# Performance work log

Hardware: AMD Instinct MI355X
Metric: run time of the kernel (lower is better)

Reference implementation:

```python
import jax, jax.numpy as jnp
import numpy as np

E = 600000
NF = 50000
NC = 12500
D = 128
HID = 128
D_IN = 4 * D  # concat of four gathered feature blocks


def setup_inputs() -> dict:
    key = jax.random.key(0)
    ks = jax.random.split(key, 10)
    return {
        "h_dk_coarse": jax.random.normal(ks[0], (NC, D), dtype=jnp.float32),
        "h_si_fine": jax.random.normal(ks[1], (NF, D), dtype=jnp.float32),
        "h_sk_coarse": jax.random.normal(ks[2], (NC, D), dtype=jnp.float32),
        "h_di_fine_current": jax.random.normal(ks[3], (NF, D), dtype=jnp.float32),
        "fine_idx": jax.random.randint(ks[4], (E,), 0, NF, dtype=jnp.int64),
        "coarse_idx": jax.random.randint(ks[5], (E,), 0, NC, dtype=jnp.int64),
        # Dense params (Glorot-ish scale); both layers use relu per create_mlp
        "W1": jax.random.normal(ks[6], (D_IN, HID), dtype=jnp.float32) * (1.0 / np.sqrt(D_IN)),
        "b1": jnp.zeros((HID,), dtype=jnp.float32),
        "W2": jax.random.normal(ks[7], (HID, D), dtype=jnp.float32) * (1.0 / np.sqrt(HID)),
        "b2": jnp.zeros((D,), dtype=jnp.float32),
    }


def reference(h_dk_coarse, h_si_fine, h_sk_coarse, h_di_fine_current,
              fine_idx, coarse_idx, W1, b1, W2, b2):
    # Gather per-edge features
    h_dk_g = h_dk_coarse[coarse_idx]          # [E, D]
    h_si_g = h_si_fine[fine_idx]              # [E, D]
    h_sk_g = h_sk_coarse[coarse_idx]          # [E, D]
    h_di_g = h_di_fine_current[fine_idx]      # [E, D]
    x = jnp.concatenate([h_si_g, h_sk_g, h_di_g, h_dk_g], axis=-1)  # [E, 4D]
    # MLP: relu on hidden AND final layer (create_mlp default activation, no final override)
    h = jax.nn.relu(x @ W1 + b1)              # [E, HID]
    psi = jax.nn.relu(h @ W2 + b2)            # [E, D]
    contributions = psi * h_dk_g              # [E, D]
    # Scatter-add back to fine nodes
    return jax.ops.segment_sum(contributions, fine_idx, num_segments=NF)  # [NF, D]
```

## Files before the change

### kernel.cpp

```cpp
#include <hip/hip_runtime.h>

typedef unsigned char u8;
typedef unsigned short u16;
typedef unsigned int u32;

#define E_EDGES 600000
#define NUM_FINE 50000
#define NUM_COARSE 12500
#define FINE_BLOCKS 391
#define COARSE_BLOCKS 98
#define CONVERT_BLOCKS 320
#define HCONV_BLOCKS 782
#define COUNT_BLOCKS 2344
#define SCATTER_BLOCKS 2344
#define ZOUT_BLOCKS 625
#define PADF 53248
#define SCAN_BLOCKS 196

typedef __attribute__((ext_vector_type(8))) short short8;
typedef __attribute__((ext_vector_type(4))) float f32x4;

union Frag { short8 v; u16 s[8]; u32 u[4]; uint4 q; };

__device__ __forceinline__ u32 rne_bf16(float f) {
  union { float f; u32 u; } v; v.f = f;
  return (v.u + 0x7FFFu + ((v.u >> 16) & 1u)) >> 16;
}
__device__ __forceinline__ float hi_bf(u32 u) {
  union { u32 x; float f; } v; v.x = u & 0xFFFF0000u; return v.f;
}
__device__ __forceinline__ float lo_bf(u32 u) {
  union { u32 x; float f; } v; v.x = u << 16; return v.f;
}
__device__ __forceinline__ float up_bf(u16 u) {
  union { u32 x; float f; } v; v.x = ((u32)u) << 16; return v.f;
}
__device__ __forceinline__ u32 pack_trunc(float hi, float lo) {
  union { float f; u32 x; } a, b; a.f = hi; b.f = lo;
  return __builtin_amdgcn_perm(a.x, b.x, 0x07060302u);
}
__device__ __forceinline__ u32 addrelu_pack(u32 a, u32 b) {
  float lo = fmaxf(lo_bf(a) + lo_bf(b), 0.0f);
  float hi = fmaxf(hi_bf(a) + hi_bf(b), 0.0f);
  return pack_trunc(hi, lo);
}
__device__ __forceinline__ u16 trunc_bf16(float f) {
  union { float f; u32 u; } v; v.f = f;
  return (u16)(v.u >> 16);
}
__device__ __forceinline__ u32 rne_pack(float lo, float hi) {
  return rne_bf16(lo) | (rne_bf16(hi) << 16);
}

__global__ void prep1(const float* __restrict__ W1, const float* __restrict__ W2,
                      u16* __restrict__ BW1f, u16* __restrict__ BW1c,
                      u16* __restrict__ BW2,
                      const float* __restrict__ h_dk, u16* __restrict__ Hc,
                      const int* __restrict__ fidx, u32* __restrict__ cnt4,
                      u8* __restrict__ rk) {
  if (blockIdx.x < CONVERT_BLOCKS) {
    int o = blockIdx.x * 256 + threadIdx.x;
    if (o >= 81920) return;
    int which = (o < 32768) ? 0 : (o < 65536 ? 1 : 2);
    int idx = (which == 2) ? (o - 65536) : (o & 32767);
    int j = idx & 7, lane = (idx >> 3) & 63, nt = (idx >> 9) & 7, ks = idx >> 12;
    int k = ks * 32 + (lane >> 4) * 8 + j;
    int n = nt * 16 + (lane & 15);
    float v;
    if (which == 2) v = W2[k * 128 + n];
    else {
      int row;
      if (which == 0) row = (k < 128) ? k : (256 + (k - 128));
      else            row = (k < 128) ? (128 + k) : (384 + (k - 128));
      v = W1[row * 128 + n];
    }
    u16 b = (u16)rne_bf16(v);
    if (which == 0) BW1f[idx] = b; else if (which == 1) BW1c[idx] = b; else BW2[idx] = b;
  } else if (blockIdx.x < CONVERT_BLOCKS + HCONV_BLOCKS) {
    int t = (blockIdx.x - CONVERT_BLOCKS) * 256 + threadIdx.x;
    if (t < (NUM_COARSE * 128) / 8) {
      const float4* s = (const float4*)(h_dk + t * 8);
      float4 v0 = s[0], v1 = s[1];
      uint4 o;
      o.x = rne_pack(v0.x, v0.y);
      o.y = rne_pack(v0.z, v0.w);
      o.z = rne_pack(v1.x, v1.y);
      o.w = rne_pack(v1.z, v1.w);
      *(uint4*)(Hc + t * 8) = o;
    }
  } else {
    int e = (blockIdx.x - CONVERT_BLOCKS - HCONV_BLOCKS) * 256 + threadIdx.x;
    if (e < E_EDGES) {
      int fi = fidx[e];
      u32 r = atomicAdd(&cnt4[(e & 3) * PADF + fi], 1u);
      rk[e] = (u8)r;
    }
  }
}

__global__ void scan1(const u32* __restrict__ cnt4, u32* __restrict__ roots) {
  __shared__ u32 wsum[4];
  const int tid = threadIdx.x, lane = tid & 63, w = tid >> 6;
  const int fi = blockIdx.x * 256 + tid;
  u32 tot = 0;
  if (fi < NUM_FINE)
    tot = cnt4[fi] + cnt4[PADF + fi] + cnt4[2 * PADF + fi] + cnt4[3 * PADF + fi];
  u32 x = tot;
#pragma unroll
  for (int off = 32; off >= 1; off >>= 1) x += __shfl_down(x, off, 64);
  if (lane == 0) wsum[w] = x;
  __syncthreads();
  if (tid == 0) roots[blockIdx.x] = wsum[0] + wsum[1] + wsum[2] + wsum[3];
}

__global__ void scan2(u32* __restrict__ cnt4, const u32* __restrict__ roots) {
  __shared__ u32 wsum[4], wred[4];
  __shared__ u32 sh_bbase;
  const int tid = threadIdx.x, lane = tid & 63, w = tid >> 6;
  const int fi = blockIdx.x * 256 + tid;

  u32 c0 = 0, c1 = 0, c2 = 0, c3 = 0;
  if (fi < NUM_FINE) {
    c0 = cnt4[fi];            c1 = cnt4[PADF + fi];
    c2 = cnt4[2 * PADF + fi]; c3 = cnt4[3 * PADF + fi];
  }
  const u32 tot = c0 + c1 + c2 + c3;

  u32 rv = (tid < (int)blockIdx.x && tid < SCAN_BLOCKS) ? roots[tid] : 0;
#pragma unroll
  for (int off = 32; off >= 1; off >>= 1) rv += __shfl_down(rv, off, 64);
  if (lane == 0) wred[w] = rv;
  __syncthreads();
  if (tid == 0) sh_bbase = wred[0] + wred[1] + wred[2] + wred[3];

  u32 xi = tot;
#pragma unroll
  for (int off = 1; off < 64; off <<= 1) {
    u32 y = __shfl_up(xi, off, 64);
    if (lane >= off) xi += y;
  }
  if (lane == 63) wsum[w] = xi;
  __syncthreads();
  u32 woffs = 0;
  for (int k = 0; k < w; ++k) woffs += wsum[k];
  const u32 g = sh_bbase + woffs + xi - tot;

  if (fi < NUM_FINE) {
    cnt4[fi] = g;
    cnt4[PADF + fi] = g + c0;
    cnt4[2 * PADF + fi] = g + c0 + c1;
    cnt4[3 * PADF + fi] = g + c0 + c1 + c2;
  }
}

__global__ __launch_bounds__(256, 2) void prep2(
    const int* __restrict__ fidx, const int* __restrict__ cidx,
    const u32* __restrict__ base4, const u8* __restrict__ rk,
    u32* __restrict__ spk, float* __restrict__ out,
    const float* __restrict__ h_dk, const float* __restrict__ h_si,
    const float* __restrict__ h_sk, const float* __restrict__ h_di,
    const u16* __restrict__ BW1f, const u16* __restrict__ BW1c,
    const float* __restrict__ b1, u16* __restrict__ Pf, u16* __restrict__ Pc) {
  __shared__ u16 bsh[32768];

  if (blockIdx.x < SCATTER_BLOCKS) {
    int e = blockIdx.x * 256 + threadIdx.x;
    if (e < E_EDGES) {
      int fi = fidx[e];
      u32 pos = base4[(e & 3) * PADF + fi] + rk[e];
      spk[pos] = ((u32)fi << 14) | (u32)cidx[e];
    }
    return;
  }
  if (blockIdx.x < SCATTER_BLOCKS + ZOUT_BLOCKS) {
    const int zb = blockIdx.x - SCATTER_BLOCKS;
    float4* o4 = (float4*)out;
    const float4 z = {0.f, 0.f, 0.f, 0.f};
    int idx = zb * 2560 + threadIdx.x;
#pragma unroll
    for (int i = 0; i < 10; ++i) o4[idx + i * 256] = z;
    return;
  }

  const int b = blockIdx.x - SCATTER_BLOCKS - ZOUT_BLOCKS;
  const bool fine = b < FINE_BLOCKS;
  const int rowStart = fine ? b * 128 : (b - FINE_BLOCKS) * 128;
  const int R = fine ? NUM_FINE : NUM_COARSE;
  const float* __restrict__ X1 = fine ? h_si : h_sk;
  const float* __restrict__ X2 = fine ? h_di : h_dk;
  const u16* __restrict__ BW = fine ? BW1f : BW1c;
  u16* __restrict__ P = fine ? Pf : Pc;

  const int tid = threadIdx.x;
  {
    uint4* d4 = (uint4*)bsh;
    const uint4* s4 = (const uint4*)BW;
#pragma unroll
    for (int k = 0; k < 16; ++k) d4[k * 256 + tid] = s4[k * 256 + tid];
  }
  __syncthreads();

  const int lane = tid & 63;
  const int w = tid >> 6;
  const int qd = lane >> 4;
  const int ml = lane & 15;

  int rowA[2]; bool vA[2];
#pragma unroll
  for (int mt = 0; mt < 2; ++mt) {
    rowA[mt] = rowStart + w * 32 + mt * 16 + ml;
    vA[mt] = rowA[mt] < R;
  }

  f32x4 acc[2][8];
#pragma unroll
  for (int mt = 0; mt < 2; ++mt)
#pragma unroll
    for (int nt = 0; nt < 8; ++nt) acc[mt][nt] = (f32x4){0.f, 0.f, 0.f, 0.f};

  for (int ks = 0; ks < 8; ++ks) {
    const int k0 = ks * 32 + qd * 8;
    short8 a[2];
#pragma unroll
    for (int mt = 0; mt < 2; ++mt) {
      Frag af;
      if (vA[mt]) {
        const float* src = (k0 < 128) ? (X1 + rowA[mt] * 128 + k0)
                                      : (X2 + rowA[mt] * 128 + (k0 - 128));
        const float4* s4 = (const float4*)src;
        float4 v0 = s4[0], v1 = s4[1];
        af.u[0] = pack_trunc(v0.y, v0.x);
        af.u[1] = pack_trunc(v0.w, v0.z);
        af.u[2] = pack_trunc(v1.y, v1.x);
        af.u[3] = pack_trunc(v1.w, v1.z);
      } else {
        af.u[0] = af.u[1] = af.u[2] = af.u[3] = 0u;
      }
      a[mt] = af.v;
    }
#pragma unroll
    for (int nt = 0; nt < 8; ++nt) {
      Frag bfr;
      bfr.q = *(const uint4*)&bsh[(((ks * 8 + nt) * 64) + lane) * 8];
      acc[0][nt] = __builtin_amdgcn_mfma_f32_16x16x32_bf16(a[0], bfr.v, acc[0][nt], 0, 0, 0);
      acc[1][nt] = __builtin_amdgcn_mfma_f32_16x16x32_bf16(a[1], bfr.v, acc[1][nt], 0, 0, 0);
    }
  }

  float b1v[8];
#pragma unroll
  for (int nt = 0; nt < 8; ++nt) b1v[nt] = fine ? 0.0f : b1[nt * 16 + ml];

#pragma unroll
  for (int mt = 0; mt < 2; ++mt) {
#pragma unroll
    for (int r = 0; r < 4; ++r) {
      const int row = rowStart + w * 32 + mt * 16 + qd * 4 + r;
      if (row < R) {
#pragma unroll
        for (int nt = 0; nt < 8; ++nt)
          P[row * 128 + nt * 16 + ml] = (u16)rne_bf16(acc[mt][nt][r] + b1v[nt]);
      }
    }
  }
}

__global__ __launch_bounds__(256, 4) void edge_kernel(
    const u16* __restrict__ Pf, const u16* __restrict__ Pc,
    const u16* __restrict__ BW2, const u16* __restrict__ Hc,
    const u32* __restrict__ spk, const float* __restrict__ b2,
    float* __restrict__ out) {
  __shared__ u16 smem[16384];
  __shared__ int sh_fi[128], sh_ci[128], sh_segstart[130];
  __shared__ int shS, shHead, shTail, shW0tot;

  const int tid = threadIdx.x;
  const int eb = blockIdx.x * 128;
  const int V = min(128, E_EDGES - eb);

  {
    uint4* d4 = (uint4*)smem;
    const uint4* s4 = (const uint4*)BW2;
#pragma unroll
    for (int k = 0; k < 8; ++k) d4[k * 256 + tid] = s4[k * 256 + tid];
  }
  if (tid < 128) {
    if (tid < V) {
      u32 p = spk[eb + tid];
      sh_fi[tid] = (int)(p >> 14);
      sh_ci[tid] = (int)(p & 16383u);
    } else { sh_fi[tid] = -1; sh_ci[tid] = 0; }
  }
  if (tid == 0) {
    shHead = (eb > 0) ? (int)(spk[eb - 1] >> 14) : -1;
    shTail = (eb + V < E_EDGES) ? (int)(spk[eb + V] >> 14) : -1;
  }
  __syncthreads();

  int f = 0, x = 0;
  if (tid < 128) {
    f = (tid < V) ? ((tid == 0) ? 1 : (sh_fi[tid] != sh_fi[tid - 1] ? 1 : 0)) : 0;
    x = f;
#pragma unroll
    for (int off = 1; off < 64; off <<= 1) {
      int y = __shfl_up(x, off, 64);
      if ((tid & 63) >= off) x += y;
    }
  }
  if (tid == 63) shW0tot = x;
  __syncthreads();
  if (tid >= 64 && tid < 128) x += shW0tot;
  if (tid < V) {
    if (f) sh_segstart[x - 1] = tid;
    if (tid == V - 1) { shS = x; sh_segstart[x] = V; }
  }
  __syncthreads();

  const int lane = tid & 63;
  const int w = tid >> 6;
  const int qd = lane >> 4;
  const int ml = lane & 15;

  int fiA[2], ciA[2]; bool vA[2];
#pragma unroll
  for (int mt = 0; mt < 2; ++mt) {
    const int lr = w * 32 + mt * 16 + ml;
    vA[mt] = lr < V;
    fiA[mt] = vA[mt] ? sh_fi[lr] : 0;
    ciA[mt] = vA[mt] ? sh_ci[lr] : 0;
  }

  f32x4 acc[2][8];
#pragma unroll
  for (int mt = 0; mt < 2; ++mt)
#pragma unroll
    for (int nt = 0; nt < 8; ++nt) acc[mt][nt] = (f32x4){0.f, 0.f, 0.f, 0.f};

  for (int ks = 0; ks < 4; ++ks) {
    const int k0 = ks * 32 + qd * 8;
    short8 a[2];
#pragma unroll
    for (int mt = 0; mt < 2; ++mt) {
      Frag af;
      if (vA[mt]) {
        uint4 pf = *(const uint4*)(Pf + fiA[mt] * 128 + k0);
        uint4 pc = *(const uint4*)(Pc + ciA[mt] * 128 + k0);
        af.u[0] = addrelu_pack(pf.x, pc.x);
        af.u[1] = addrelu_pack(pf.y, pc.y);
        af.u[2] = addrelu_pack(pf.z, pc.z);
        af.u[3] = addrelu_pack(pf.w, pc.w);
      } else {
        af.u[0] = af.u[1] = af.u[2] = af.u[3] = 0u;
      }
      a[mt] = af.v;
    }
#pragma unroll
    for (int nt = 0; nt < 8; ++nt) {
      Frag bfr;
      bfr.q = *(const uint4*)&smem[(((ks * 8 + nt) * 64) + lane) * 8];
      acc[0][nt] = __builtin_amdgcn_mfma_f32_16x16x32_bf16(a[0], bfr.v, acc[0][nt], 0, 0, 0);
      acc[1][nt] = __builtin_amdgcn_mfma_f32_16x16x32_bf16(a[1], bfr.v, acc[1][nt], 0, 0, 0);
    }
  }
  __syncthreads();

  float b2v[8];
#pragma unroll
  for (int nt = 0; nt < 8; ++nt) b2v[nt] = b2[nt * 16 + ml];

#pragma unroll
  for (int mt = 0; mt < 2; ++mt) {
#pragma unroll
    for (int r = 0; r < 4; ++r) {
      const int lr = w * 32 + mt * 16 + qd * 4 + r;
      if (lr < V) {
        const u16* __restrict__ hrow = Hc + sh_ci[lr] * 128;
#pragma unroll
        for (int nt = 0; nt < 8; ++nt) {
          const int col = nt * 16 + ml;
          const float psi = fmaxf(acc[mt][nt][r] + b2v[nt], 0.0f);
          smem[lr * 128 + col] = trunc_bf16(psi * up_bf(hrow[col]));
        }
      }
    }
  }
  __syncthreads();

  const int S = shS;
  for (int idx = tid; idx < S * 64; idx += 256) {
    const int s = idx >> 6, cp = idx & 63;
    const int r0 = sh_segstart[s], r1 = sh_segstart[s + 1];
    float a0 = 0.f, a1 = 0.f;
    for (int r = r0; r < r1; ++r) {
      const u32 v = *(const u32*)&smem[r * 128 + cp * 2];
      a0 += lo_bf(v);
      a1 += hi_bf(v);
    }
    const int fi = sh_fi[r0];
    float* op = out + (size_t)fi * 128 + cp * 2;
    const bool at = (s == 0 && shHead == fi) || (s == S - 1 && shTail == fi);
    if (at) { atomicAdd(op, a0); atomicAdd(op + 1, a1); }
    else { op[0] = a0; op[1] = a1; }
  }
}

extern "C" void kernel_launch(void* const* d_in, const int* in_sizes, int n_in,
                              void* d_out, int out_size, void* d_ws, size_t ws_size,
                              hipStream_t stream) {
  const float* h_dk = (const float*)d_in[0];
  const float* h_si = (const float*)d_in[1];
  const float* h_sk = (const float*)d_in[2];
  const float* h_di = (const float*)d_in[3];
  const int* fidx = (const int*)d_in[4];
  const int* cidx = (const int*)d_in[5];
  const float* W1 = (const float*)d_in[6];
  const float* b1 = (const float*)d_in[7];
  const float* W2 = (const float*)d_in[8];
  const float* b2 = (const float*)d_in[9];
  float* out = (float*)d_out;

  u16* Pf   = (u16*)d_ws;
  u16* Pc   = Pf + (size_t)NUM_FINE * 128;
  u16* BW1f = Pc + (size_t)NUM_COARSE * 128;
  u16* BW1c = BW1f + 32768;
  u16* BW2  = BW1c + 32768;
  u16* Hc   = BW2 + 16384;
  u32* cnt4 = (u32*)(Hc + (size_t)NUM_COARSE * 128);
  u32* spk  = cnt4 + 4 * PADF;
  u8*  rk   = (u8*)(spk + E_EDGES);
  u32* roots = (u32*)(rk + E_EDGES);

  hipMemsetAsync(cnt4, 0, 4 * PADF * sizeof(u32), stream);

  prep1<<<CONVERT_BLOCKS + HCONV_BLOCKS + COUNT_BLOCKS, 256, 0, stream>>>(
      W1, W2, BW1f, BW1c, BW2, h_dk, Hc, fidx, cnt4, rk);
  scan1<<<SCAN_BLOCKS, 256, 0, stream>>>(cnt4, roots);
  scan2<<<SCAN_BLOCKS, 256, 0, stream>>>(cnt4, roots);
  prep2<<<SCATTER_BLOCKS + ZOUT_BLOCKS + FINE_BLOCKS + COARSE_BLOCKS, 256, 0, stream>>>(
      fidx, cidx, cnt4, rk, spk, out, h_dk, h_si, h_sk, h_di,
      BW1f, BW1c, b1, Pf, Pc);
  edge_kernel<<<(E_EDGES + 127) / 128, 256, 0, stream>>>(
      Pf, Pc, BW2, Hc, spk, b2, out);
}
```

Baseline: 239.7 us.

## Move node-level GEMM into first kernel and convert W1 in-block

The per-node W1 projection (Pf/Pc) now runs in the first launch alongside the edge-count atomics and h_dk/W2 conversion, instead of after the scan in prep2. Each GEMM block converts its own half of W1 to bf16 into shared memory rather than reading a pre-converted copy, which drops a dependency stage and halves the shared-memory footprint. Counter copies for the atomic histogram grow from 4 to 8 to reduce contention. The cost is redundant W1 conversion in every GEMM block and more counter traffic in the scans.

```diff
diff --git a/kernel.cpp b/kernel.cpp
--- a/kernel.cpp
+++ b/kernel.cpp
@@ -9,12 +9,14 @@
 #define NUM_COARSE 12500
 #define FINE_BLOCKS 391
 #define COARSE_BLOCKS 98
-#define CONVERT_BLOCKS 320
+#define COUNT_BLOCKS 2344
+#define PRE_BLOCKS (FINE_BLOCKS + COARSE_BLOCKS)
 #define HCONV_BLOCKS 782
-#define COUNT_BLOCKS 2344
+#define W2CONV_BLOCKS 64
 #define SCATTER_BLOCKS 2344
 #define ZOUT_BLOCKS 625
 #define PADF 53248
+#define NCOPY 8
 #define SCAN_BLOCKS 196
 
 typedef __attribute__((ext_vector_type(8))) short short8;
@@ -52,153 +54,58 @@
   return rne_bf16(lo) | (rne_bf16(hi) << 16);
 }
 
-__global__ void prep1(const float* __restrict__ W1, const float* __restrict__ W2,
-                      u16* __restrict__ BW1f, u16* __restrict__ BW1c,
-                      u16* __restrict__ BW2,
-                      const float* __restrict__ h_dk, u16* __restrict__ Hc,
-                      const int* __restrict__ fidx, u32* __restrict__ cnt4,
-                      u8* __restrict__ rk) {
-  if (blockIdx.x < CONVERT_BLOCKS) {
-    int o = blockIdx.x * 256 + threadIdx.x;
-    if (o >= 81920) return;
-    int which = (o < 32768) ? 0 : (o < 65536 ? 1 : 2);
-    int idx = (which == 2) ? (o - 65536) : (o & 32767);
-    int j = idx & 7, lane = (idx >> 3) & 63, nt = (idx >> 9) & 7, ks = idx >> 12;
-    int k = ks * 32 + (lane >> 4) * 8 + j;
-    int n = nt * 16 + (lane & 15);
-    float v;
-    if (which == 2) v = W2[k * 128 + n];
-    else {
-      int row;
-      if (which == 0) row = (k < 128) ? k : (256 + (k - 128));
-      else            row = (k < 128) ? (128 + k) : (384 + (k - 128));
-      v = W1[row * 128 + n];
-    }
-    u16 b = (u16)rne_bf16(v);
-    if (which == 0) BW1f[idx] = b; else if (which == 1) BW1c[idx] = b; else BW2[idx] = b;
-  } else if (blockIdx.x < CONVERT_BLOCKS + HCONV_BLOCKS) {
-    int t = (blockIdx.x - CONVERT_BLOCKS) * 256 + threadIdx.x;
-    if (t < (NUM_COARSE * 128) / 8) {
-      const float4* s = (const float4*)(h_dk + t * 8);
-      float4 v0 = s[0], v1 = s[1];
-      uint4 o;
-      o.x = rne_pack(v0.x, v0.y);
-      o.y = rne_pack(v0.z, v0.w);
-      o.z = rne_pack(v1.x, v1.y);
-      o.w = rne_pack(v1.z, v1.w);
-      *(uint4*)(Hc + t * 8) = o;
-    }
-  } else {
-    int e = (blockIdx.x - CONVERT_BLOCKS - HCONV_BLOCKS) * 256 + threadIdx.x;
+__global__ __launch_bounds__(256, 2) void mega1(
+    const int* __restrict__ fidx, u32* __restrict__ cnt8, u8* __restrict__ rk,
+    const float* __restrict__ h_dk, const float* __restrict__ h_si,
+    const float* __restrict__ h_sk, const float* __restrict__ h_di,
+    const float* __restrict__ W1, const float* __restrict__ W2,
+    const float* __restrict__ b1,
+    u16* __restrict__ Pf, u16* __restrict__ Pc,
+    u16* __restrict__ Hc, u16* __restrict__ BW2) {
+  __shared__ u16 bsh[16384];
+
+  const int tid = threadIdx.x;
+
+  if (blockIdx.x < COUNT_BLOCKS) {
+    int e = blockIdx.x * 256 + tid;
     if (e < E_EDGES) {
       int fi = fidx[e];
-      u32 r = atomicAdd(&cnt4[(e & 3) * PADF + fi], 1u);
+      u32 r = atomicAdd(&cnt8[(e & 7) * PADF + fi], 1u);
       rk[e] = (u8)r;
     }
-  }
-}
-
-__global__ void scan1(const u32* __restrict__ cnt4, u32* __restrict__ roots) {
-  __shared__ u32 wsum[4];
-  const int tid = threadIdx.x, lane = tid & 63, w = tid >> 6;
-  const int fi = blockIdx.x * 256 + tid;
-  u32 tot = 0;
-  if (fi < NUM_FINE)
-    tot = cnt4[fi] + cnt4[PADF + fi] + cnt4[2 * PADF + fi] + cnt4[3 * PADF + fi];
-  u32 x = tot;
-#pragma unroll
-  for (int off = 32; off >= 1; off >>= 1) x += __shfl_down(x, off, 64);
-  if (lane == 0) wsum[w] = x;
-  __syncthreads();
-  if (tid == 0) roots[blockIdx.x] = wsum[0] + wsum[1] + wsum[2] + wsum[3];
-}
-
-__global__ void scan2(u32* __restrict__ cnt4, const u32* __restrict__ roots) {
-  __shared__ u32 wsum[4], wred[4];
-  __shared__ u32 sh_bbase;
-  const int tid = threadIdx.x, lane = tid & 63, w = tid >> 6;
-  const int fi = blockIdx.x * 256 + tid;
-
-  u32 c0 = 0, c1 = 0, c2 = 0, c3 = 0;
-  if (fi < NUM_FINE) {
-    c0 = cnt4[fi];            c1 = cnt4[PADF + fi];
-    c2 = cnt4[2 * PADF + fi]; c3 = cnt4[3 * PADF + fi];
-  }
-  const u32 tot = c0 + c1 + c2 + c3;
-
-  u32 rv = (tid < (int)blockIdx.x && tid < SCAN_BLOCKS) ? roots[tid] : 0;
-#pragma unroll
-  for (int off = 32; off >= 1; off >>= 1) rv += __shfl_down(rv, off, 64);
-  if (lane == 0) wred[w] = rv;
-  __syncthreads();
-  if (tid == 0) sh_bbase = wred[0] + wred[1] + wred[2] + wred[3];
-
-  u32 xi = tot;
-#pragma unroll
-  for (int off = 1; off < 64; off <<= 1) {
-    u32 y = __shfl_up(xi, off, 64);
-    if (lane >= off) xi += y;
-  }
-  if (lane == 63) wsum[w] = xi;
-  __syncthreads();
-  u32 woffs = 0;
-  for (int k = 0; k < w; ++k) woffs += wsum[k];
-  const u32 g = sh_bbase + woffs + xi - tot;
-
-  if (fi < NUM_FINE) {
-    cnt4[fi] = g;
-    cnt4[PADF + fi] = g + c0;
-    cnt4[2 * PADF + fi] = g + c0 + c1;
-    cnt4[3 * PADF + fi] = g + c0 + c1 + c2;
-  }
-}
-
-__global__ __launch_bounds__(256, 2) void prep2(
-    const int* __restrict__ fidx, const int* __restrict__ cidx,
-    const u32* __restrict__ base4, const u8* __restrict__ rk,
-    u32* __restrict__ spk, float* __restrict__ out,
-    const float* __restrict__ h_dk, const float* __restrict__ h_si,
-    const float* __restrict__ h_sk, const float* __restrict__ h_di,
-    const u16* __restrict__ BW1f, const u16* __restrict__ BW1c,
-    const float* __restrict__ b1, u16* __restrict__ Pf, u16* __restrict__ Pc) {
-  __shared__ u16 bsh[32768];
-
-  if (blockIdx.x < SCATTER_BLOCKS) {
-    int e = blockIdx.x * 256 + threadIdx.x;
-    if (e < E_EDGES) {
-      int fi = fidx[e];
-      u32 pos = base4[(e & 3) * PADF + fi] + rk[e];
-      spk[pos] = ((u32)fi << 14) | (u32)cidx[e];
-    }
     return;
   }
-  if (blockIdx.x < SCATTER_BLOCKS + ZOUT_BLOCKS) {
-    const int zb = blockIdx.x - SCATTER_BLOCKS;
-    float4* o4 = (float4*)out;
-    const float4 z = {0.f, 0.f, 0.f, 0.f};
-    int idx = zb * 2560 + threadIdx.x;
-#pragma unroll
-    for (int i = 0; i < 10; ++i) o4[idx + i * 256] = z;
+  if (blockIdx.x >= COUNT_BLOCKS + PRE_BLOCKS) {
+    const int bb = blockIdx.x - COUNT_BLOCKS - PRE_BLOCKS;
+    if (bb < HCONV_BLOCKS) {
+      int t = bb * 256 + tid;
+      if (t < (NUM_COARSE * 128) / 8) {
+        const float4* s = (const float4*)(h_dk + t * 8);
+        float4 v0 = s[0], v1 = s[1];
+        uint4 o;
+        o.x = rne_pack(v0.x, v0.y);
+        o.y = rne_pack(v0.z, v0.w);
+        o.z = rne_pack(v1.x, v1.y);
+        o.w = rne_pack(v1.z, v1.w);
+        *(uint4*)(Hc + t * 8) = o;
+      }
+    } else {
+      int idx = (bb - HCONV_BLOCKS) * 256 + tid;
+      int j = idx & 7, lane = (idx >> 3) & 63, nt = (idx >> 9) & 7, ks = idx >> 12;
+      int k = ks * 32 + (lane >> 4) * 8 + j;
+      int n = nt * 16 + (lane & 15);
+      BW2[idx] = (u16)rne_bf16(W2[k * 128 + n]);
+    }
     return;
   }
 
-  const int b = blockIdx.x - SCATTER_BLOCKS - ZOUT_BLOCKS;
+  const int b = blockIdx.x - COUNT_BLOCKS;
   const bool fine = b < FINE_BLOCKS;
   const int rowStart = fine ? b * 128 : (b - FINE_BLOCKS) * 128;
   const int R = fine ? NUM_FINE : NUM_COARSE;
   const float* __restrict__ X1 = fine ? h_si : h_sk;
   const float* __restrict__ X2 = fine ? h_di : h_dk;
-  const u16* __restrict__ BW = fine ? BW1f : BW1c;
   u16* __restrict__ P = fine ? Pf : Pc;
-
-  const int tid = threadIdx.x;
-  {
-    uint4* d4 = (uint4*)bsh;
-    const uint4* s4 = (const uint4*)BW;
-#pragma unroll
-    for (int k = 0; k < 16; ++k) d4[k * 256 + tid] = s4[k * 256 + tid];
-  }
-  __syncthreads();
 
   const int lane = tid & 63;
   const int w = tid >> 6;
@@ -218,33 +125,55 @@
 #pragma unroll
     for (int nt = 0; nt < 8; ++nt) acc[mt][nt] = (f32x4){0.f, 0.f, 0.f, 0.f};
 
-  for (int ks = 0; ks < 8; ++ks) {
-    const int k0 = ks * 32 + qd * 8;
-    short8 a[2];
-#pragma unroll
-    for (int mt = 0; mt < 2; ++mt) {
-      Frag af;
-      if (vA[mt]) {
-        const float* src = (k0 < 128) ? (X1 + rowA[mt] * 128 + k0)
-                                      : (X2 + rowA[mt] * 128 + (k0 - 128));
-        const float4* s4 = (const float4*)src;
-        float4 v0 = s4[0], v1 = s4[1];
-        af.u[0] = pack_trunc(v0.y, v0.x);
-        af.u[1] = pack_trunc(v0.w, v0.z);
-        af.u[2] = pack_trunc(v1.y, v1.x);
-        af.u[3] = pack_trunc(v1.w, v1.z);
-      } else {
-        af.u[0] = af.u[1] = af.u[2] = af.u[3] = 0u;
-      }
-      a[mt] = af.v;
-    }
-#pragma unroll
-    for (int nt = 0; nt < 8; ++nt) {
-      Frag bfr;
-      bfr.q = *(const uint4*)&bsh[(((ks * 8 + nt) * 64) + lane) * 8];
-      acc[0][nt] = __builtin_amdgcn_mfma_f32_16x16x32_bf16(a[0], bfr.v, acc[0][nt], 0, 0, 0);
-      acc[1][nt] = __builtin_amdgcn_mfma_f32_16x16x32_bf16(a[1], bfr.v, acc[1][nt], 0, 0, 0);
-    }
+  for (int half = 0; half < 2; ++half) {
+    {
+      const int kl = tid >> 1;
+      const int nh = (tid & 1) * 64;
+      const int wrow = (fine ? 0 : 128) + half * 256 + kl;
+      const float4* __restrict__ src = (const float4*)(W1 + wrow * 128 + nh);
+      const int ksl = kl >> 5, kqd = (kl >> 3) & 3, j = kl & 7;
+#pragma unroll 4
+      for (int g4 = 0; g4 < 16; ++g4) {
+        float4 v = src[g4];
+        const int n = nh + g4 * 4;
+        const int nt = n >> 4;
+        u16* dst = &bsh[(((ksl * 8 + nt) * 64) + kqd * 16 + (n & 15)) * 8 + j];
+        dst[0]  = (u16)rne_bf16(v.x);
+        dst[8]  = (u16)rne_bf16(v.y);
+        dst[16] = (u16)rne_bf16(v.z);
+        dst[24] = (u16)rne_bf16(v.w);
+      }
+    }
+    __syncthreads();
+
+    const float* __restrict__ X = half ? X2 : X1;
+    for (int ksl = 0; ksl < 4; ++ksl) {
+      const int k0 = ksl * 32 + qd * 8;
+      short8 a[2];
+#pragma unroll
+      for (int mt = 0; mt < 2; ++mt) {
+        Frag af;
+        if (vA[mt]) {
+          const float4* s4 = (const float4*)(X + rowA[mt] * 128 + k0);
+          float4 v0 = s4[0], v1 = s4[1];
+          af.u[0] = pack_trunc(v0.y, v0.x);
+          af.u[1] = pack_trunc(v0.w, v0.z);
+          af.u[2] = pack_trunc(v1.y, v1.x);
+          af.u[3] = pack_trunc(v1.w, v1.z);
+        } else {
+          af.u[0] = af.u[1] = af.u[2] = af.u[3] = 0u;
+        }
+        a[mt] = af.v;
+      }
+#pragma unroll
+      for (int nt = 0; nt < 8; ++nt) {
+        Frag bfr;
+        bfr.q = *(const uint4*)&bsh[(((ksl * 8 + nt) * 64) + lane) * 8];
+        acc[0][nt] = __builtin_amdgcn_mfma_f32_16x16x32_bf16(a[0], bfr.v, acc[0][nt], 0, 0, 0);
+        acc[1][nt] = __builtin_amdgcn_mfma_f32_16x16x32_bf16(a[1], bfr.v, acc[1][nt], 0, 0, 0);
+      }
+    }
+    __syncthreads();
   }
 
   float b1v[8];
@@ -262,6 +191,82 @@
           P[row * 128 + nt * 16 + ml] = (u16)rne_bf16(acc[mt][nt][r] + b1v[nt]);
       }
     }
+  }
+}
+
+__global__ void scan1(const u32* __restrict__ cnt8, u32* __restrict__ roots) {
+  __shared__ u32 wsum[4];
+  const int tid = threadIdx.x, lane = tid & 63, w = tid >> 6;
+  const int fi = blockIdx.x * 256 + tid;
+  u32 tot = 0;
+  if (fi < NUM_FINE) {
+#pragma unroll
+    for (int c = 0; c < NCOPY; ++c) tot += cnt8[c * PADF + fi];
+  }
+  u32 x = tot;
+#pragma unroll
+  for (int off = 32; off >= 1; off >>= 1) x += __shfl_down(x, off, 64);
+  if (lane == 0) wsum[w] = x;
+  __syncthreads();
+  if (tid == 0) roots[blockIdx.x] = wsum[0] + wsum[1] + wsum[2] + wsum[3];
+}
+
+__global__ void scan2(u32* __restrict__ cnt8, const u32* __restrict__ roots) {
+  __shared__ u32 wsum[4], wred[4];
+  __shared__ u32 sh_bbase;
+  const int tid = threadIdx.x, lane = tid & 63, w = tid >> 6;
+  const int fi = blockIdx.x * 256 + tid;
+
+  u32 c[NCOPY];
+  u32 tot = 0;
+#pragma unroll
+  for (int i = 0; i < NCOPY; ++i) {
+    c[i] = (fi < NUM_FINE) ? cnt8[i * PADF + fi] : 0;
+    tot += c[i];
+  }
+
+  u32 rv = (tid < (int)blockIdx.x && tid < SCAN_BLOCKS) ? roots[tid] : 0;
+#pragma unroll
+  for (int off = 32; off >= 1; off >>= 1) rv += __shfl_down(rv, off, 64);
+  if (lane == 0) wred[w] = rv;
+  __syncthreads();
+  if (tid == 0) sh_bbase = wred[0] + wred[1] + wred[2] + wred[3];
+
+  u32 xi = tot;
+#pragma unroll
+  for (int off = 1; off < 64; off <<= 1) {
+    u32 y = __shfl_up(xi, off, 64);
+    if (lane >= off) xi += y;
+  }
+  if (lane == 63) wsum[w] = xi;
+  __syncthreads();
+  u32 woffs = 0;
+  for (int k = 0; k < w; ++k) woffs += wsum[k];
+  u32 g = sh_bbase + woffs + xi - tot;
+
+  if (fi < NUM_FINE) {
+#pragma unroll
+    for (int i = 0; i < NCOPY; ++i) { cnt8[i * PADF + fi] = g; g += c[i]; }
+  }
+}
+
+__global__ void scatterz(const int* __restrict__ fidx, const int* __restrict__ cidx,
+                         const u32* __restrict__ base8, const u8* __restrict__ rk,
+                         u32* __restrict__ spk, float* __restrict__ out) {
+  if (blockIdx.x < SCATTER_BLOCKS) {
+    int e = blockIdx.x * 256 + threadIdx.x;
+    if (e < E_EDGES) {
+      int fi = fidx[e];
+      u32 pos = base8[(e & 7) * PADF + fi] + rk[e];
+      spk[pos] = ((u32)fi << 14) | (u32)cidx[e];
+    }
+  } else {
+    const int zb = blockIdx.x - SCATTER_BLOCKS;
+    float4* o4 = (float4*)out;
+    const float4 z = {0.f, 0.f, 0.f, 0.f};
+    int idx = zb * 2560 + threadIdx.x;
+#pragma unroll
+    for (int i = 0; i < 10; ++i) o4[idx + i * 256] = z;
   }
 }
 
@@ -421,24 +426,21 @@
 
   u16* Pf   = (u16*)d_ws;
   u16* Pc   = Pf + (size_t)NUM_FINE * 128;
-  u16* BW1f = Pc + (size_t)NUM_COARSE * 128;
-  u16* BW1c = BW1f + 32768;
-  u16* BW2  = BW1c + 32768;
+  u16* BW2  = Pc + (size_t)NUM_COARSE * 128;
   u16* Hc   = BW2 + 16384;
-  u32* cnt4 = (u32*)(Hc + (size_t)NUM_COARSE * 128);
-  u32* spk  = cnt4 + 4 * PADF;
+  u32* cnt8 = (u32*)(Hc + (size_t)NUM_COARSE * 128);
+  u32* spk  = cnt8 + NCOPY * PADF;
   u8*  rk   = (u8*)(spk + E_EDGES);
   u32* roots = (u32*)(rk + E_EDGES);
 
-  hipMemsetAsync(cnt4, 0, 4 * PADF * sizeof(u32), stream);
-
-  prep1<<<CONVERT_BLOCKS + HCONV_BLOCKS + COUNT_BLOCKS, 256, 0, stream>>>(
-      W1, W2, BW1f, BW1c, BW2, h_dk, Hc, fidx, cnt4, rk);
-  scan1<<<SCAN_BLOCKS, 256, 0, stream>>>(cnt4, roots);
-  scan2<<<SCAN_BLOCKS, 256, 0, stream>>>(cnt4, roots);
-  prep2<<<SCATTER_BLOCKS + ZOUT_BLOCKS + FINE_BLOCKS + COARSE_BLOCKS, 256, 0, stream>>>(
-      fidx, cidx, cnt4, rk, spk, out, h_dk, h_si, h_sk, h_di,
-      BW1f, BW1c, b1, Pf, Pc);
+  hipMemsetAsync(cnt8, 0, NCOPY * PADF * sizeof(u32), stream);
+
+  mega1<<<COUNT_BLOCKS + PRE_BLOCKS + HCONV_BLOCKS + W2CONV_BLOCKS, 256, 0, stream>>>(
+      fidx, cnt8, rk, h_dk, h_si, h_sk, h_di, W1, W2, b1, Pf, Pc, Hc, BW2);
+  scan1<<<SCAN_BLOCKS, 256, 0, stream>>>(cnt8, roots);
+  scan2<<<SCAN_BLOCKS, 256, 0, stream>>>(cnt8, roots);
+  scatterz<<<SCATTER_BLOCKS + ZOUT_BLOCKS, 256, 0, stream>>>(
+      fidx, cidx, cnt8, rk, spk, out);
   edge_kernel<<<(E_EDGES + 127) / 128, 256, 0, stream>>>(
       Pf, Pc, BW2, Hc, spk, b2, out);
 }
```

Result: slower. 252.8 us (+5.5%).
